# Performance work log

Hardware: AMD Instinct MI355X
Metric: run time of the kernel (lower is better)

Reference implementation:

```python
import jax, jax.numpy as jnp
import numpy as np

N = 10000      # nodes
E = 160000     # edges
MUL = 16       # multiplicity of 0e and 1o irreps
NB = 16        # num radial basis
H = 64         # radial MLP hidden
WN = 4 * MUL * MUL  # tensor-product weight_numel (4 CG paths, uvw weights)


def setup_inputs() -> dict:
    key = jax.random.key(0)
    ks = jax.random.split(key, 10)
    node_features = jax.random.normal(ks[0], (N, 4 * MUL), dtype=jnp.float32)  # [N, 16 + 16*3]
    edge_index = jax.random.randint(ks[1], (2, E), 0, N)
    edge_sh = jax.random.normal(ks[2], (E, 4), dtype=jnp.float32)              # 1x0e + 1x1o
    edge_radial_emb = jax.random.uniform(ks[3], (E, NB), dtype=jnp.float32)
    # RadialMLP params
    w1 = jax.random.normal(ks[4], (NB, H), dtype=jnp.float32) / np.sqrt(NB).astype(np.float32)
    b1 = jnp.zeros((H,), jnp.float32)
    w2 = jax.random.normal(ks[5], (H, WN), dtype=jnp.float32) / np.sqrt(H).astype(np.float32)
    b2 = jnp.zeros((WN,), jnp.float32)
    # equivariant Linear params (one [mul,mul] mix per irrep)
    lin_w0 = jax.random.normal(ks[6], (MUL, MUL), dtype=jnp.float32)
    lin_w1 = jax.random.normal(ks[7], (MUL, MUL), dtype=jnp.float32)
    return dict(node_features=node_features, edge_sh=edge_sh, edge_radial_emb=edge_radial_emb,
                w1=w1, b1=b1, w2=w2, b2=b2, lin_w0=lin_w0, lin_w1=lin_w1,
                edge_index=edge_index)


def reference(node_features, edge_sh, edge_radial_emb, w1, b1, w2, b2, lin_w0, lin_w1, edge_index):
    n = node_features.shape[0]
    src, dst = edge_index[0], edge_index[1]
    # radial MLP -> per-edge tensor-product weights, split into the 4 CG paths
    tpw = jax.nn.silu(edge_radial_emb @ w1 + b1) @ w2 + b2        # [E, 4*MUL*MUL]
    W = tpw.reshape(-1, 4, MUL, MUL)
    W00, W01, W10, W11 = W[:, 0], W[:, 1], W[:, 2], W[:, 3]
    # gather source node features, split into scalar (0e) and vector (1o) parts
    xf = node_features[src]
    xs = xf[:, :MUL]                                              # [E, MUL]
    xv = xf[:, MUL:].reshape(-1, MUL, 3)                          # [E, MUL, 3]
    shs = edge_sh[:, 0:1]                                         # [E, 1]
    shv = edge_sh[:, 1:4]                                         # [E, 3]
    alpha = np.float32(1.0 / np.sqrt(2.0 * MUL))  # path norm: 2 paths feed each output irrep
    inv_sqrt3 = np.float32(1.0 / np.sqrt(3.0))    # w3j(1,1,0) contraction constant
    # scalar messages: 0e*0e->0e and 1o*1o->0e
    msg_s = alpha * (jnp.einsum('eu,euv->ev', xs * shs, W00)
                     + inv_sqrt3 * jnp.einsum('eui,ei,euv->ev', xv, shv, W11))
    # vector messages: 0e*1o->1o and 1o*0e->1o
    msg_v = alpha * (jnp.einsum('eu,euv,ei->evi', xs, W01, shv)
                     + jnp.einsum('eui,euv->evi', xv * shs[:, :, None], W10))
    # scatter-sum messages into destination nodes
    agg_s = jax.ops.segment_sum(msg_s, dst, num_segments=n)       # [N, MUL]
    agg_v = jax.ops.segment_sum(msg_v, dst, num_segments=n)       # [N, MUL, 3]
    # equivariant linear (channel mixing per irrep, 1/sqrt(fan_in) norm)
    s = np.float32(1.0 / np.sqrt(MUL))
    ts = (agg_s @ lin_w0) * s
    tv = jnp.einsum('nui,uv->nvi', agg_v, lin_w1) * s
    # NormActivation: x * silu(||x||)/||x||
    eps = np.float32(1e-8)
    ns = jnp.abs(ts)
    act_s = ts * (jax.nn.silu(ns) / (ns + eps))
    nv = jnp.sqrt(jnp.sum(tv * tv, axis=-1))
    act_v = tv * (jax.nn.silu(nv) / (nv + eps))[..., None]
    # identity skip (input irreps == output irreps)
    return node_features + jnp.concatenate([act_s, act_v.reshape(n, MUL * 3)], axis=-1)
```

## Files before the change

### kernel.cpp

```cpp
#include <hip/hip_runtime.h>
#include <hip/hip_bf16.h>
#include <math.h>

#define EPB 64
#define ALPHA 0.17677669529663687f
#define INV_SQRT3 0.57735026918962576f

typedef __attribute__((ext_vector_type(8))) short short8;
typedef __attribute__((ext_vector_type(4))) float f32x4;

__device__ __forceinline__ float silu_f(float x) { return x / (1.0f + __expf(-x)); }

__device__ __forceinline__ unsigned short bf16_rne(float x) {
  unsigned int u = __float_as_uint(x);
  unsigned int r = u + 0x7fffu + ((u >> 16) & 1u);
  return (unsigned short)(r >> 16);
}

__global__ __launch_bounds__(256) void prep_kernel(const float* __restrict__ w2,
                                                   unsigned short* __restrict__ w2t,
                                                   const int* __restrict__ eidx,
                                                   int* __restrict__ deg,
                                                   int* __restrict__ rank, int E) {
  if (blockIdx.x < 16) {
    __shared__ unsigned short tile[16][260];
    const int t = threadIdx.x;
    const int k0 = (blockIdx.x & 3) * 16;
    const int c0 = (blockIdx.x >> 2) * 256;
    #pragma unroll
    for (int j = 0; j < 16; ++j)
      tile[j][t] = bf16_rne(w2[(size_t)(k0 + j) * 1024 + c0 + t]);
    __syncthreads();
    union { unsigned short s[16]; uint4 q[2]; } pk;
    #pragma unroll
    for (int j = 0; j < 16; ++j) pk.s[j] = tile[j][t];
    uint4* dst = (uint4*)&w2t[(size_t)(c0 + t) * 64 + k0];
    dst[0] = pk.q[0];
    dst[1] = pk.q[1];
  } else {
    const int e = (blockIdx.x - 16) * 256 + threadIdx.x;
    if (e < E) rank[e] = atomicAdd(&deg[eidx[E + e]], 1);
  }
}

__global__ __launch_bounds__(1024) void scan_kernel(const int* __restrict__ deg,
                                                    int* __restrict__ offs, int N) {
  __shared__ int sums[1024];
  const int t = threadIdx.x;
  const int ch = (N + 1023) >> 10;
  const int lo = t * ch;
  const int hi = min(lo + ch, N);
  int s = 0;
  for (int i = lo; i < hi; ++i) s += deg[i];
  sums[t] = s;
  __syncthreads();
  #pragma unroll
  for (int d = 1; d < 1024; d <<= 1) {
    int v = (t >= d) ? sums[t - d] : 0;
    __syncthreads();
    sums[t] += v;
    __syncthreads();
  }
  int run = sums[t] - s;
  for (int i = lo; i < hi; ++i) { offs[i] = run; run += deg[i]; }
  if (lo < N && hi == N) offs[N] = run;
}

__global__ __launch_bounds__(256, 3) void tfn_edge_kernel(
    const float* __restrict__ nf,
    const float* __restrict__ esh,
    const float* __restrict__ emb,
    const float* __restrict__ w1g,
    const float* __restrict__ b1g,
    const unsigned short* __restrict__ w2t,
    const float* __restrict__ b2g,
    const int*   __restrict__ eidx,
    const int*   __restrict__ rank,
    const int*   __restrict__ offs,
    float* __restrict__ msg,
    float* __restrict__ agg,
    int E, int posmode)
{
  __shared__ __align__(16) unsigned char smem[42336];
  float* fsT  = (float*)(smem);
  float* fbT  = (float*)(smem + 4352);
  float* fxvT = (float*)(smem + 8704);
  unsigned short* embs = (unsigned short*)(smem + 21760);
  unsigned short* w1T  = (unsigned short*)(smem + 23808);
  float* t01 = (float*)(smem);
  float* t2s = (float*)(smem + 9216);
  float* t3s = (float*)(smem + 13824);
  unsigned short* hsm = (unsigned short*)(smem + 27744);
  float* b2s   = (float*)(smem + 36960);
  float* shs_l = (float*)(smem + 41056);
  float* shv_l = (float*)(smem + 41312);
  int*   pos_l = (int*)(smem + 42080);

  const int tid = threadIdx.x;
  const int ebase = blockIdx.x * EPB;

  {
    const int e = tid >> 2, p = tid & 3;
    int eg = ebase + e; if (eg >= E) eg = E - 1;

    const float4 em = *(const float4*)&emb[(size_t)eg * 16 + p * 4];
    {
      const unsigned int lo = bf16_rne(em.x) | ((unsigned int)bf16_rne(em.y) << 16);
      const unsigned int hi = bf16_rne(em.z) | ((unsigned int)bf16_rne(em.w) << 16);
      *(uint2*)&embs[e * 16 + p * 4] = make_uint2(lo, hi);
    }

    const float4 sh = *(const float4*)&esh[(size_t)eg * 4];
    if (p == 0) {
      shs_l[e] = sh.x;
      shv_l[e * 3 + 0] = sh.y; shv_l[e * 3 + 1] = sh.z; shv_l[e * 3 + 2] = sh.w;
      const int dst = eidx[E + eg];
      pos_l[e] = posmode ? (offs[dst] + rank[eg]) : dst;
    }

    const int src = eidx[eg];
    const float4* row4 = (const float4*)(nf + (size_t)src * 64);
    const float4 xs4 = row4[p];
    const float4 va  = row4[4 + p * 3 + 0];
    const float4 vb  = row4[4 + p * 3 + 1];
    const float4 vc  = row4[4 + p * 3 + 2];
    const float xsr[4] = {xs4.x, xs4.y, xs4.z, xs4.w};
    const float xvf[12] = {va.x, va.y, va.z, va.w, vb.x, vb.y, vb.z, vb.w,
                           vc.x, vc.y, vc.z, vc.w};
    #pragma unroll
    for (int uu = 0; uu < 4; ++uu) {
      const int u = p * 4 + uu;
      const float x0 = xvf[uu * 3 + 0];
      const float x1 = xvf[uu * 3 + 1];
      const float x2 = xvf[uu * 3 + 2];
      fsT[u * 68 + e] = xsr[uu];
      fbT[u * 68 + e] = x0 * sh.y + x1 * sh.z + x2 * sh.w;
      fxvT[0 * 1088 + u * 68 + e] = x0;
      fxvT[1 * 1088 + u * 68 + e] = x1;
      fxvT[2 * 1088 + u * 68 + e] = x2;
    }
  }
  {
    const int r = tid >> 4, c4 = (tid & 15) * 4;
    const float4 wv = *(const float4*)&w1g[r * 64 + c4];
    w1T[(c4 + 0) * 16 + r] = bf16_rne(wv.x);
    w1T[(c4 + 1) * 16 + r] = bf16_rne(wv.y);
    w1T[(c4 + 2) * 16 + r] = bf16_rne(wv.z);
    w1T[(c4 + 3) * 16 + r] = bf16_rne(wv.w);
  }
  *(float4*)&b2s[tid * 4] = *(const float4*)&b2g[tid * 4];
  __syncthreads();

  const int lane = tid & 63;
  const int sec  = tid >> 6;
  const int q = lane >> 4, m = lane & 15;

  union AF { uint4 u4; short8 s8; };

  {
    AF ea;
    if (q < 2) ea.u4 = *(const uint4*)&embs[(sec * 16 + m) * 16 + q * 8];
    else       ea.u4 = make_uint4(0, 0, 0, 0);
    #pragma unroll
    for (int ct = 0; ct < 4; ++ct) {
      AF wb;
      if (q < 2) wb.u4 = *(const uint4*)&w1T[(ct * 16 + m) * 16 + q * 8];
      else       wb.u4 = make_uint4(0, 0, 0, 0);
      const float b1v = b1g[ct * 16 + m];
      f32x4 c = {b1v, b1v, b1v, b1v};
      c = __builtin_amdgcn_mfma_f32_16x16x32_bf16(ea.s8, wb.s8, c, 0, 0, 0);
      #pragma unroll
      for (int r = 0; r < 4; ++r)
        hsm[(sec * 16 + q * 4 + r) * 72 + ct * 16 + m] = bf16_rne(silu_f(c[r]));
    }
  }
  __syncthreads();

  AF afr[4][2];
  #pragma unroll
  for (int mt = 0; mt < 4; ++mt)
    #pragma unroll
    for (int ks = 0; ks < 2; ++ks)
      afr[mt][ks].u4 = *(const uint4*)&hsm[(mt * 16 + m) * 72 + ks * 32 + q * 8];

  const float* ftab = (sec == 3) ? fbT : fsT;
  const uint4* w2tq = (const uint4*)w2t;
  const uint4* bp = w2tq + ((size_t)(sec * 256 + m)) * 8 + q;

  float accA[4][4] = {};
  float accB[4][4] = {};
  float accC[4][4] = {};

  AF b0v, b1v;
  b0v.u4 = bp[0];
  b1v.u4 = bp[4];

  #pragma unroll 2
  for (int u = 0; u < 16; ++u) {
    AF n0, n1;
    if (u < 15) {
      n0.u4 = bp[(u + 1) * 128];
      n1.u4 = bp[(u + 1) * 128 + 4];
    }
    const float b2v = b2s[sec * 256 + u * 16 + m];

    #pragma unroll
    for (int mt = 0; mt < 4; ++mt) {
      f32x4 c = {b2v, b2v, b2v, b2v};
      c = __builtin_amdgcn_mfma_f32_16x16x32_bf16(afr[mt][0].s8, b0v.s8, c, 0, 0, 0);
      c = __builtin_amdgcn_mfma_f32_16x16x32_bf16(afr[mt][1].s8, b1v.s8, c, 0, 0, 0);

      const int fo = mt * 16 + q * 4;
      if (sec == 2) {
        const float4 f0 = *(const float4*)&fxvT[0 * 1088 + u * 68 + fo];
        const float4 f1 = *(const float4*)&fxvT[1 * 1088 + u * 68 + fo];
        const float4 f2 = *(const float4*)&fxvT[2 * 1088 + u * 68 + fo];
        const float fA[4] = {f0.x, f0.y, f0.z, f0.w};
        const float fB[4] = {f1.x, f1.y, f1.z, f1.w};
        const float fC[4] = {f2.x, f2.y, f2.z, f2.w};
        #pragma unroll
        for (int r = 0; r < 4; ++r) {
          accA[mt][r] = fmaf(fA[r], c[r], accA[mt][r]);
          accB[mt][r] = fmaf(fB[r], c[r], accB[mt][r]);
          accC[mt][r] = fmaf(fC[r], c[r], accC[mt][r]);
        }
      } else {
        const float4 f = *(const float4*)&ftab[u * 68 + fo];
        const float fA[4] = {f.x, f.y, f.z, f.w};
        #pragma unroll
        for (int r = 0; r < 4; ++r)
          accA[mt][r] = fmaf(fA[r], c[r], accA[mt][r]);
      }
    }
    if (u < 15) { b0v = n0; b1v = n1; }
  }

  __syncthreads();

  #pragma unroll
  for (int mt = 0; mt < 4; ++mt)
    #pragma unroll
    for (int r = 0; r < 4; ++r) {
      const int e = mt * 16 + q * 4 + r;
      if (sec == 0)      t01[e * 18 + m]        = accA[mt][r] * shs_l[e];
      else if (sec == 1) t2s[e * 18 + m]        = accA[mt][r];
      else if (sec == 3) t01[1152 + e * 18 + m] = accA[mt][r];
      else {
        const float s = shs_l[e];
        t3s[0 * 1160 + e * 18 + m] = accA[mt][r] * s;
        t3s[1 * 1160 + e * 18 + m] = accB[mt][r] * s;
        t3s[2 * 1160 + e * 18 + m] = accC[mt][r] * s;
      }
    }
  __syncthreads();

  {
    const int w = tid >> 6, lc = tid & 63;
    const int cc = lc - 16;
    const int v  = cc / 3;
    const int i3 = cc - v * 3;
    #pragma unroll 1
    for (int t8 = 0; t8 < 16; ++t8) {
      const int e = w * 16 + t8;
      if (ebase + e < E) {
        float val;
        if (lc < 16) {
          val = ALPHA * (t01[e * 18 + lc] + INV_SQRT3 * t01[1152 + e * 18 + lc]);
        } else {
          val = ALPHA * (t2s[e * 18 + v] * shv_l[e * 3 + i3] + t3s[i3 * 1160 + e * 18 + v]);
        }
        if (posmode) msg[(size_t)pos_l[e] * 64 + lc] = val;
        else         atomicAdd(&agg[(size_t)pos_l[e] * 64 + lc], val);
      }
    }
  }
}

__global__ __launch_bounds__(256) void tfn_agg_node_kernel(
    const float* __restrict__ msg, const int* __restrict__ offs,
    const float* __restrict__ nf, const float* __restrict__ lw0,
    const float* __restrict__ lw1, float* __restrict__ out, int N)
{
  __shared__ float ag[4 * 68];
  __shared__ float w0s[256], w1s[256];
  const int t = threadIdx.x;
  w0s[t] = lw0[t];
  w1s[t] = lw1[t];

  const int n0 = blockIdx.x * 4;
  {
    const int w = t >> 6, lane = t & 63;
    const int rq = lane >> 4, cl = lane & 15;
    const int n = n0 + w;
    if (n < N) {
      const int s = offs[n], e = offs[n + 1];
      float a0 = 0.0f, a1 = 0.0f, a2 = 0.0f, a3 = 0.0f;
      for (int j = s + rq; j < e; j += 4) {
        const float4 v = *(const float4*)&msg[(size_t)j * 64 + cl * 4];
        a0 += v.x; a1 += v.y; a2 += v.z; a3 += v.w;
      }
      a0 += __shfl_xor(a0, 16); a0 += __shfl_xor(a0, 32);
      a1 += __shfl_xor(a1, 16); a1 += __shfl_xor(a1, 32);
      a2 += __shfl_xor(a2, 16); a2 += __shfl_xor(a2, 32);
      a3 += __shfl_xor(a3, 16); a3 += __shfl_xor(a3, 32);
      if (rq == 0) *(float4*)&ag[w * 68 + cl * 4] = make_float4(a0, a1, a2, a3);
    }
  }
  __syncthreads();
  {
    const int node = t >> 6, c = t & 63;
    const int n = n0 + node;
    if (n >= N) return;
    const float* a = &ag[node * 68];
    float val;
    if (c < 16) {
      float accv = 0.0f;
      #pragma unroll
      for (int u = 0; u < 16; ++u) accv = fmaf(a[u], w0s[u * 16 + c], accv);
      const float ts = 0.25f * accv;
      const float ns = fabsf(ts);
      const float g = (ns / (1.0f + __expf(-ns))) / (ns + 1e-8f);
      val = ts * g;
    } else {
      const int cc = c - 16;
      const int v = cc / 3, i = cc - v * 3;
      float a0 = 0.0f, a1 = 0.0f, a2 = 0.0f;
      #pragma unroll
      for (int u = 0; u < 16; ++u) {
        const float w = w1s[u * 16 + v];
        a0 = fmaf(a[16 + u * 3 + 0], w, a0);
        a1 = fmaf(a[16 + u * 3 + 1], w, a1);
        a2 = fmaf(a[16 + u * 3 + 2], w, a2);
      }
      a0 *= 0.25f; a1 *= 0.25f; a2 *= 0.25f;
      const float nv = sqrtf(a0 * a0 + a1 * a1 + a2 * a2);
      const float g = (nv / (1.0f + __expf(-nv))) / (nv + 1e-8f);
      val = ((i == 0) ? a0 : (i == 1) ? a1 : a2) * g;
    }
    out[(size_t)n * 64 + c] = nf[(size_t)n * 64 + c] + val;
  }
}

__global__ __launch_bounds__(256) void tfn_node_kernel(
    const float* __restrict__ nf,
    const float* __restrict__ lw0,
    const float* __restrict__ lw1,
    float* __restrict__ out, int N)
{
  __shared__ float w0s[256], w1s[256];
  const int tid = threadIdx.x;
  w0s[tid] = lw0[tid];
  w1s[tid] = lw1[tid];
  __syncthreads();

  const int n = blockIdx.x * 256 + tid;
  if (n >= N) return;

  float* rowp = out + (size_t)n * 64;
  float as[16], av[16][3];
  #pragma unroll
  for (int u = 0; u < 16; ++u) as[u] = rowp[u];
  #pragma unroll
  for (int u = 0; u < 16; ++u) {
    av[u][0] = rowp[16 + u * 3 + 0];
    av[u][1] = rowp[16 + u * 3 + 1];
    av[u][2] = rowp[16 + u * 3 + 2];
  }
  const float* nfr = nf + (size_t)n * 64;
  float res[64];

  #pragma unroll
  for (int v = 0; v < 16; ++v) {
    float acc = 0.0f;
    #pragma unroll
    for (int u = 0; u < 16; ++u) acc = fmaf(as[u], w0s[u * 16 + v], acc);
    const float ts = 0.25f * acc;
    const float ns = fabsf(ts);
    const float g = (ns / (1.0f + __expf(-ns))) / (ns + 1e-8f);
    res[v] = nfr[v] + ts * g;
  }
  #pragma unroll
  for (int v = 0; v < 16; ++v) {
    float a0 = 0.0f, a1 = 0.0f, a2 = 0.0f;
    #pragma unroll
    for (int u = 0; u < 16; ++u) {
      const float w = w1s[u * 16 + v];
      a0 = fmaf(av[u][0], w, a0);
      a1 = fmaf(av[u][1], w, a1);
      a2 = fmaf(av[u][2], w, a2);
    }
    a0 *= 0.25f; a1 *= 0.25f; a2 *= 0.25f;
    const float nv = sqrtf(a0 * a0 + a1 * a1 + a2 * a2);
    const float g = (nv / (1.0f + __expf(-nv))) / (nv + 1e-8f);
    res[16 + v * 3 + 0] = nfr[16 + v * 3 + 0] + a0 * g;
    res[16 + v * 3 + 1] = nfr[16 + v * 3 + 1] + a1 * g;
    res[16 + v * 3 + 2] = nfr[16 + v * 3 + 2] + a2 * g;
  }
  #pragma unroll
  for (int o = 0; o < 64; o += 4) {
    *(float4*)&rowp[o] = make_float4(res[o], res[o + 1], res[o + 2], res[o + 3]);
  }
}

extern "C" void kernel_launch(void* const* d_in, const int* in_sizes, int n_in,
                              void* d_out, int out_size, void* d_ws, size_t ws_size,
                              hipStream_t stream) {
  const float* nf  = (const float*)d_in[0];
  const float* esh = (const float*)d_in[1];
  const float* emb = (const float*)d_in[2];
  const float* w1  = (const float*)d_in[3];
  const float* b1  = (const float*)d_in[4];
  const float* w2  = (const float*)d_in[5];
  const float* b2  = (const float*)d_in[6];
  const float* lw0 = (const float*)d_in[7];
  const float* lw1 = (const float*)d_in[8];
  const int*   eix = (const int*)d_in[9];

  const int N = in_sizes[0] / 64;
  const int E = in_sizes[9] / 2;
  float* out = (float*)d_out;

  char* ws = (char*)d_ws;
  const size_t o_w2t  = 0;
  const size_t o_deg  = 131072;
  const size_t o_offs = o_deg  + (((size_t)N * 4 + 15) & ~(size_t)15);
  const size_t o_rank = o_offs + (((size_t)(N + 1) * 4 + 15) & ~(size_t)15);
  const size_t o_msg  = (o_rank + (size_t)E * 4 + 255) & ~(size_t)255;
  const size_t need   = o_msg + (size_t)E * 256;
  const int posmode = (ws_size >= need) ? 1 : 0;

  unsigned short* w2t = (unsigned short*)(ws + o_w2t);
  int*   deg  = (int*)(ws + o_deg);
  int*   offs = (int*)(ws + o_offs);
  int*   rankp = (int*)(ws + o_rank);
  float* msg  = (float*)(ws + o_msg);

  const int eblocks = (E + EPB - 1) / EPB;

  if (posmode) {
    hipMemsetAsync(deg, 0, (size_t)N * 4, stream);
    prep_kernel<<<dim3(16 + (E + 255) / 256), dim3(256), 0, stream>>>(
        w2, w2t, eix, deg, rankp, E);
    scan_kernel<<<dim3(1), dim3(1024), 0, stream>>>(deg, offs, N);
    tfn_edge_kernel<<<dim3(eblocks), dim3(256), 0, stream>>>(
        nf, esh, emb, w1, b1, w2t, b2, eix, rankp, offs, msg, out, E, 1);
    tfn_agg_node_kernel<<<dim3((N + 3) / 4), dim3(256), 0, stream>>>(
        msg, offs, nf, lw0, lw1, out, N);
  } else {
    prep_kernel<<<dim3(16), dim3(256), 0, stream>>>(w2, w2t, eix, nullptr, nullptr, 0);
    hipMemsetAsync(out, 0, (size_t)out_size * sizeof(float), stream);
    tfn_edge_kernel<<<dim3(eblocks), dim3(256), 0, stream>>>(
        nf, esh, emb, w1, b1, w2t, b2, eix, nullptr, nullptr, nullptr, out, E, 0);
    tfn_node_kernel<<<dim3((N + 255) / 256), dim3(256), 0, stream>>>(nf, lw0, lw1, out, N);
  }
}
```

Baseline: 178.6 us.

## Fuse degree count, weight transpose and scan into one cooperative kernel

Replaces the memset, prep kernel and single-block scan with one cooperative-launch kernel that uses grid-wide syncs between zeroing degrees, counting edges per destination with atomics and transposing w2, and the prefix scan. The aim is to remove launch overhead and inter-kernel gaps for the CSR build. In exchange the scan now runs on 256 threads rather than 1024, the grid is fixed at 256 blocks, and grid.sync adds its own cost. A device-attribute query runs on every call.

```diff
diff --git a/kernel.cpp b/kernel.cpp
--- a/kernel.cpp
+++ b/kernel.cpp
@@ -1,6 +1,9 @@
 #include <hip/hip_runtime.h>
 #include <hip/hip_bf16.h>
+#include <hip/hip_cooperative_groups.h>
 #include <math.h>
+
+namespace cg = cooperative_groups;
 
 #define EPB 64
 #define ALPHA 0.17677669529663687f
@@ -15,6 +18,61 @@
   unsigned int u = __float_as_uint(x);
   unsigned int r = u + 0x7fffu + ((u >> 16) & 1u);
   return (unsigned short)(r >> 16);
+}
+
+__global__ __launch_bounds__(256) void csr_kernel(
+    const float* __restrict__ w2, unsigned short* __restrict__ w2t,
+    const int* __restrict__ eidx, int* __restrict__ deg,
+    int* __restrict__ rank, int* __restrict__ offs, int N, int E)
+{
+  __shared__ unsigned short tile[16][260];
+  __shared__ int sums[256];
+  cg::grid_group grid = cg::this_grid();
+  const int t = threadIdx.x;
+  const int bid = blockIdx.x;
+  const int GT = gridDim.x * 256;
+  const int gt = bid * 256 + t;
+
+  for (int i = gt; i < N; i += GT) deg[i] = 0;
+  grid.sync();
+
+  for (int e = gt; e < E; e += GT) rank[e] = atomicAdd(&deg[eidx[E + e]], 1);
+
+  if (bid < 16) {
+    const int k0 = (bid & 3) * 16;
+    const int c0 = (bid >> 2) * 256;
+    #pragma unroll
+    for (int j = 0; j < 16; ++j)
+      tile[j][t] = bf16_rne(w2[(size_t)(k0 + j) * 1024 + c0 + t]);
+    __syncthreads();
+    union { unsigned short s[16]; uint4 q[2]; } pk;
+    #pragma unroll
+    for (int j = 0; j < 16; ++j) pk.s[j] = tile[j][t];
+    uint4* dst = (uint4*)&w2t[(size_t)(c0 + t) * 64 + k0];
+    dst[0] = pk.q[0];
+    dst[1] = pk.q[1];
+  }
+  grid.sync();
+
+  if (bid == 0) {
+    const int ch = (N + 255) >> 8;
+    const int lo = t * ch;
+    const int hi = min(lo + ch, N);
+    int s = 0;
+    for (int i = lo; i < hi; ++i) s += deg[i];
+    sums[t] = s;
+    __syncthreads();
+    #pragma unroll
+    for (int d = 1; d < 256; d <<= 1) {
+      int v = (t >= d) ? sums[t - d] : 0;
+      __syncthreads();
+      sums[t] += v;
+      __syncthreads();
+    }
+    int run = sums[t] - s;
+    for (int i = lo; i < hi; ++i) { offs[i] = run; run += deg[i]; }
+    if (lo < N && hi == N) offs[N] = run;
+  }
 }
 
 __global__ __launch_bounds__(256) void prep_kernel(const float* __restrict__ w2,
@@ -437,11 +495,25 @@
 
   const int eblocks = (E + EPB - 1) / EPB;
 
+  int coop = 0, dev = 0;
+  hipGetDevice(&dev);
+  hipDeviceGetAttribute(&coop, hipDeviceAttributeCooperativeLaunch, dev);
+
   if (posmode) {
-    hipMemsetAsync(deg, 0, (size_t)N * 4, stream);
-    prep_kernel<<<dim3(16 + (E + 255) / 256), dim3(256), 0, stream>>>(
-        w2, w2t, eix, deg, rankp, E);
-    scan_kernel<<<dim3(1), dim3(1024), 0, stream>>>(deg, offs, N);
+    if (coop) {
+      const float* w2a = w2;
+      const int* eixa = eix;
+      int Na = N, Ea = E;
+      void* args[] = {(void*)&w2a, (void*)&w2t, (void*)&eixa, (void*)&deg,
+                      (void*)&rankp, (void*)&offs, (void*)&Na, (void*)&Ea};
+      hipLaunchCooperativeKernel((void*)csr_kernel, dim3(256), dim3(256),
+                                 args, 0, stream);
+    } else {
+      hipMemsetAsync(deg, 0, (size_t)N * 4, stream);
+      prep_kernel<<<dim3(16 + (E + 255) / 256), dim3(256), 0, stream>>>(
+          w2, w2t, eix, deg, rankp, E);
+      scan_kernel<<<dim3(1), dim3(1024), 0, stream>>>(deg, offs, N);
+    }
     tfn_edge_kernel<<<dim3(eblocks), dim3(256), 0, stream>>>(
         nf, esh, emb, w1, b1, w2t, b2, eix, rankp, offs, msg, out, E, 1);
     tfn_agg_node_kernel<<<dim3((N + 3) / 4), dim3(256), 0, stream>>>(
```

Measured after the change: 259.8 us. 45.5% more time.
